# Performance work log

Hardware: AMD Instinct MI355X
Metric: run time of the kernel (lower is better)

## Reference

```python
import jax, jax.numpy as jnp
import numpy as np

B, QL, KL, D, H = 2, 512, 8192, 1024, 8
HD = D // H  # head dim = 128


def setup_inputs() -> dict:
    key = jax.random.key(0)
    ks = jax.random.split(key, 12)
    s = 0.02
    return {
        "inputs_q": jax.random.normal(ks[0], (B, QL, D), jnp.float32),
        "inputs_k": jax.random.normal(ks[1], (B, KL, D), jnp.float32),
        "inputs_v": jax.random.normal(ks[2], (B, KL, D), jnp.float32),
        "attention_mask": jax.random.randint(ks[3], (B, QL, KL), 0, 2).astype(bool),
        "Wq": jax.random.normal(ks[4], (D, D), jnp.float32) * s,
        "bq": jnp.zeros((D,), jnp.float32),
        "Wk": jax.random.normal(ks[5], (D, D), jnp.float32) * s,
        "bk": jnp.zeros((D,), jnp.float32),
        "Wv": jax.random.normal(ks[6], (D, D), jnp.float32) * s,
        "bv": jnp.zeros((D,), jnp.float32),
        "Wf": jax.random.normal(ks[7], (D, D), jnp.float32) * s,
        "bf": jnp.zeros((D,), jnp.float32),
    }


def reference(inputs_q, inputs_k, inputs_v, attention_mask, Wq, bq, Wk, bk, Wv, bv, Wf, bf):
    # Projections (torch Linear: x @ W.T + b)
    q = inputs_q @ Wq.T + bq  # [B, QL, D]
    k = inputs_k @ Wk.T + bk  # [B, KL, D]
    v = inputs_v @ Wv.T + bv  # [B, KL, D]

    q = q.reshape(B, QL, H, HD)
    k = k.reshape(B, KL, H, HD)
    v = v.reshape(B, KL, H, HD)

    # scores [B, H, QL, KL]
    scores = jnp.einsum("bqhd,bkhd->bhqk", q, k)
    scale = 1.0 / np.sqrt(HD).astype(np.float32)
    scores = scores * scale
    large_k = jnp.float32(1e30)
    scores = jnp.where(attention_mask[:, None, :, :], scores, -large_k)

    probs = jax.nn.softmax(scores, axis=-1)
    # note: original calls self.dropout(normalized) but discards the result -> no-op

    summed = jnp.einsum("bhqk,bkhd->bqhd", probs, v).reshape(B, QL, H * HD)

    # wipe rows whose mask is all zero
    wipe = jnp.all(~attention_mask, axis=2, keepdims=True)  # [B, QL, 1]
    summed = jnp.where(wipe, jnp.zeros_like(summed), summed)

    return summed @ Wf.T + bf
```

## Files before the change

### kernel.cpp

```cpp
#include <hip/hip_runtime.h>
#include <hip/hip_bf16.h>
#include <math.h>

typedef __attribute__((ext_vector_type(4))) float fx4;
typedef __attribute__((ext_vector_type(4))) short sx4;
typedef __attribute__((ext_vector_type(8))) short sx8;
typedef unsigned long long u64;

#define MFMA16(a, b, c) __builtin_amdgcn_mfma_f32_16x16x16bf16_1k(a, b, c, 0, 0, 0)
#define MFMA32(a, b, c) __builtin_amdgcn_mfma_f32_16x16x32_bf16(a, b, c, 0, 0, 0)

__device__ __forceinline__ unsigned short f2bf(float f) {
  unsigned int u = __float_as_uint(f);
  return (unsigned short)((u + 0x7fffu + ((u >> 16) & 1u)) >> 16);
}

__device__ __forceinline__ unsigned cvtpk(float lo, float hi) {
  unsigned r;
  asm("v_cvt_pk_bf16_f32 %0, %1, %2" : "=v"(r) : "v"(lo), "v"(hi));
  return r;
}

typedef const __attribute__((address_space(1))) char* gc1p;
typedef __attribute__((address_space(3))) char* lc3p;
__device__ __forceinline__ void glds16(const void* g, const void* lds_uniform) {
  gc1p gp = (gc1p)(unsigned long long)(uintptr_t)g;
  lc3p lp = (lc3p)(unsigned)__builtin_amdgcn_readfirstlane((int)(unsigned)(uintptr_t)lds_uniform);
  __builtin_amdgcn_global_load_lds(gp, lp, 16, 0, 0);
}

__global__ __launch_bounds__(256) void k_prep(
    const float* __restrict__ Wq, const float* __restrict__ Wk,
    const float* __restrict__ Wv, const float* __restrict__ Wf,
    const int* __restrict__ mask, short* cwq, short* cwk, short* cwv,
    short* cwf, u64* __restrict__ mb) {
  __shared__ unsigned char nib[4][256];
  const int bx = blockIdx.x;
  const int t = threadIdx.x;
  if (bx >= 256) {
    const int mrow0 = (bx - 256) * 4;
#pragma unroll
    for (int j = 0; j < 4; j++) {
      const int4 m = *(const int4*)(mask + (size_t)(mrow0 + j) * 1024 + t * 4);
      nib[j][t] = (unsigned char)((m.x != 0) | ((m.y != 0) << 1) |
                                  ((m.z != 0) << 2) | ((m.w != 0) << 3));
    }
    __syncthreads();
    if (t < 64) {
      const int j = t >> 4, i = t & 15;
      u64 wv = 0;
#pragma unroll
      for (int k = 0; k < 16; k++)
        wv |= (u64)(nib[j][i * 16 + k] & 0xF) << (4 * k);
      mb[(size_t)(mrow0 + j) * 16 + i] = wv;
    }
    return;
  }
  const int seg = bx >> 6;
  const float* s = seg == 0 ? Wq : seg == 1 ? Wk : seg == 2 ? Wv : Wf;
  short* d = seg == 0 ? cwq : seg == 1 ? cwk : seg == 2 ? cwv : cwf;
  const size_t base = (size_t)(bx & 63) * 16384;
#pragma unroll
  for (int it = 0; it < 4; it++) {
    const size_t i = base + (size_t)it * 4096 + (size_t)t * 16;
    const fx4 a0 = *(const fx4*)(s + i);
    const fx4 a1 = *(const fx4*)(s + i + 4);
    const fx4 a2 = *(const fx4*)(s + i + 8);
    const fx4 a3 = *(const fx4*)(s + i + 12);
    sx8 o0, o1;
    o0[0] = (short)f2bf(a0[0]); o0[1] = (short)f2bf(a0[1]);
    o0[2] = (short)f2bf(a0[2]); o0[3] = (short)f2bf(a0[3]);
    o0[4] = (short)f2bf(a1[0]); o0[5] = (short)f2bf(a1[1]);
    o0[6] = (short)f2bf(a1[2]); o0[7] = (short)f2bf(a1[3]);
    o1[0] = (short)f2bf(a2[0]); o1[1] = (short)f2bf(a2[1]);
    o1[2] = (short)f2bf(a2[2]); o1[3] = (short)f2bf(a2[3]);
    o1[4] = (short)f2bf(a3[0]); o1[5] = (short)f2bf(a3[1]);
    o1[6] = (short)f2bf(a3[2]); o1[7] = (short)f2bf(a3[3]);
    *(sx8*)(d + i) = o0;
    *(sx8*)(d + i + 8) = o1;
  }
}

template <int MODE, int MT, int AF32>
__device__ __forceinline__ void gemm_body(short* sA, short* sB,
                                          const void* __restrict__ Aptr,
                                          const short* __restrict__ Bw,
                                          const float* __restrict__ bias,
                                          void* __restrict__ Cptr, int M, int N,
                                          int K, float alpha, int bx) {
  const int t = threadIdx.x;
  const int lane = t & 63;
  const int w = t >> 6;
  const int quad = lane >> 4;
  const int l16 = lane & 15;
  const int x7 = l16 & 7;
  int m0, n0;
  if (M >= 8192) {
    const int ml = bx & 7, nn = (bx >> 3) & 7, mh = bx >> 6;
    m0 = (mh * 8 + ml) * MT;
    n0 = nn << 7;
  } else {
    const int ntile = N >> 7;
    n0 = (bx % ntile) << 7;
    m0 = (bx / ntile) * MT;
  }
  constexpr int NI = (MT == 128) ? 4 : 2;
  constexpr int NJ = (MT == 128) ? 4 : 2;
  const int wm = (MT == 128) ? ((w >> 1) << 6) : 0;
  const int wn = (MT == 128) ? ((w & 1) << 6) : (w << 5);
  const fx4 fzero = {0.f, 0.f, 0.f, 0.f};
  fx4 acc[4][NI];
#pragma unroll
  for (int i = 0; i < 4; i++)
#pragma unroll
    for (int j = 0; j < NI; j++) acc[i][j] = fzero;

  const int srow = lane >> 3;
  const int scb = lane & 7;
  const float* Af = (const float*)Aptr;
  const short* Ab = (const short*)Aptr;
  fx4 ra[NJ][2];

  if (AF32) {
#pragma unroll
    for (int j = 0; j < NJ; j++) {
      const int rbase = (MT == 128) ? (w * 32 + j * 8) : (j * 32 + w * 8);
      const int row = rbase + srow;
      const int cb = scb ^ (row & 7);
      const float* src = Af + (size_t)(m0 + row) * K + cb * 8;
      ra[j][0] = *(const fx4*)src;
      ra[j][1] = *(const fx4*)(src + 4);
    }
  } else {
#pragma unroll
    for (int j = 0; j < NJ; j++) {
      const int rbase = (MT == 128) ? (w * 32 + j * 8) : (j * 32 + w * 8);
      const int row = rbase + srow;
      const int cb = scb ^ (row & 7);
      glds16(Ab + (size_t)(m0 + row) * K + cb * 8, &sA[rbase * 64]);
    }
  }
#pragma unroll
  for (int j = 0; j < 4; j++) {
    const int row = w * 32 + j * 8 + srow;
    const int cb = scb ^ (row & 7);
    glds16(Bw + (size_t)(n0 + row) * K + cb * 8, &sB[(w * 32 + j * 8) * 64]);
  }
  if (AF32) {
#pragma unroll
    for (int j = 0; j < NJ; j++) {
      const int rbase = (MT == 128) ? (w * 32 + j * 8) : (j * 32 + w * 8);
      sx8 o;
      unsigned* ou = (unsigned*)&o;
      ou[0] = cvtpk(ra[j][0][0], ra[j][0][1]);
      ou[1] = cvtpk(ra[j][0][2], ra[j][0][3]);
      ou[2] = cvtpk(ra[j][1][0], ra[j][1][1]);
      ou[3] = cvtpk(ra[j][1][2], ra[j][1][3]);
      *(sx8*)(&sA[rbase * 64 + lane * 8]) = o;
    }
  }
  __syncthreads();

  int buf = 0;
  for (int k0 = 0; k0 < K; k0 += 64) {
    const int nb = buf ^ 1;
    const bool more = (k0 + 64 < K);
    if (more) {
#pragma unroll
      for (int j = 0; j < 4; j++) {
        const int row = w * 32 + j * 8 + srow;
        const int cb = scb ^ (row & 7);
        glds16(Bw + (size_t)(n0 + row) * K + (k0 + 64) + cb * 8,
               &sB[nb * 8192 + (w * 32 + j * 8) * 64]);
      }
      if (AF32) {
#pragma unroll
        for (int j = 0; j < NJ; j++) {
          const int rbase = (MT == 128) ? (w * 32 + j * 8) : (j * 32 + w * 8);
          const int row = rbase + srow;
          const int cb = scb ^ (row & 7);
          const float* src = Af + (size_t)(m0 + row) * K + (k0 + 64) + cb * 8;
          ra[j][0] = *(const fx4*)src;
          ra[j][1] = *(const fx4*)(src + 4);
        }
      } else {
#pragma unroll
        for (int j = 0; j < NJ; j++) {
          const int rbase = (MT == 128) ? (w * 32 + j * 8) : (j * 32 + w * 8);
          const int row = rbase + srow;
          const int cb = scb ^ (row & 7);
          glds16(Ab + (size_t)(m0 + row) * K + (k0 + 64) + cb * 8,
                 &sA[nb * 8192 + rbase * 64]);
        }
      }
    }
    const short* pA = sA + buf * 8192;
    const short* pB = sB + buf * 8192;
#pragma unroll
    for (int kc = 0; kc < 2; kc++) {
      const int cbp = ((kc * 4 + quad) ^ x7) * 8;
      sx8 fa[4], fb[NI];
#pragma unroll
      for (int i = 0; i < 4; i++)
        fa[i] = *(const sx8*)(&pA[(wm + i * 16 + l16) * 64 + cbp]);
#pragma unroll
      for (int i = 0; i < NI; i++)
        fb[i] = *(const sx8*)(&pB[(wn + i * 16 + l16) * 64 + cbp]);
#pragma unroll
      for (int mi = 0; mi < 4; mi++)
#pragma unroll
        for (int ni = 0; ni < NI; ni++)
          acc[mi][ni] = MFMA32(fa[mi], fb[ni], acc[mi][ni]);
    }
    if (AF32 && more) {
#pragma unroll
      for (int j = 0; j < NJ; j++) {
        const int rbase = (MT == 128) ? (w * 32 + j * 8) : (j * 32 + w * 8);
        sx8 o;
        unsigned* ou = (unsigned*)&o;
        ou[0] = cvtpk(ra[j][0][0], ra[j][0][1]);
        ou[1] = cvtpk(ra[j][0][2], ra[j][0][3]);
        ou[2] = cvtpk(ra[j][1][0], ra[j][1][1]);
        ou[3] = cvtpk(ra[j][1][2], ra[j][1][3]);
        *(sx8*)(&sA[nb * 8192 + rbase * 64 + lane * 8]) = o;
      }
    }
    __syncthreads();
    buf = nb;
  }
#pragma unroll
  for (int ni = 0; ni < NI; ni++) {
    const int col = n0 + wn + ni * 16 + l16;
    const float bval = bias[col];
    if (MODE == 2) {
#pragma unroll
      for (int mi = 0; mi < 4; mi++) {
        const int rowb = m0 + wm + mi * 16 + quad * 4;
        const int bb = rowb >> 13;
        const int kl = (rowb & 8191) ^ ((col & 8) ? 4 : 0);
        sx4 pkv;
#pragma unroll
        for (int r = 0; r < 4; r++) pkv[r] = (short)f2bf(acc[mi][ni][r] + bval);
        *(sx4*)((unsigned short*)Cptr + ((size_t)bb * 1024 + col) * 8192 + kl) = pkv;
      }
    } else {
#pragma unroll
      for (int mi = 0; mi < 4; mi++)
#pragma unroll
        for (int r = 0; r < 4; r++) {
          const int row = m0 + wm + mi * 16 + quad * 4 + r;
          const float v = (acc[mi][ni][r] + bval) * alpha;
          if (MODE == 1) ((float*)Cptr)[(size_t)row * N + col] = v;
          else ((unsigned short*)Cptr)[(size_t)row * N + col] = f2bf(v);
        }
    }
  }
}

__global__ __launch_bounds__(256) void k_proj(
    const float* __restrict__ ink, const short* __restrict__ cwk,
    const float* __restrict__ bk, short* __restrict__ Kp,
    const float* __restrict__ inv, const short* __restrict__ cwv,
    const float* __restrict__ bv, short* __restrict__ Vt,
    const float* __restrict__ inq, const short* __restrict__ cwq,
    const float* __restrict__ bq, short* __restrict__ Qp, float alpha_q) {
  __shared__ __align__(16) short smem[32768];
  const int bx = blockIdx.x;
  if (bx < 1024)
    gemm_body<0, 128, 1>(smem, smem + 16384, ink, cwk, bk, Kp, 16384, 1024,
                         1024, 1.f, bx);
  else if (bx < 2048)
    gemm_body<2, 128, 1>(smem, smem + 16384, inv, cwv, bv, Vt, 16384, 1024,
                         1024, 1.f, bx - 1024);
  else
    gemm_body<0, 64, 1>(smem, smem + 16384, inq, cwq, bq, Qp, 1024, 1024, 1024,
                        alpha_q, bx - 2048);
}

__global__ __launch_bounds__(256) void k_gemm_out(const short* __restrict__ summed,
                                                  const short* __restrict__ cwf,
                                                  const float* __restrict__ bf,
                                                  float* __restrict__ out) {
  __shared__ __align__(16) short smem[32768];
  gemm_body<1, 64, 0>(smem, smem + 16384, summed, cwf, bf, out, 1024, 1024,
                      1024, 1.f, blockIdx.x);
}

__global__ __launch_bounds__(256, 4) void k_attn(const short* __restrict__ Qp,
                                                 const short* __restrict__ Kp,
                                                 const short* __restrict__ Vt,
                                                 const u64* __restrict__ mb,
                                                 float* __restrict__ ml,
                                                 float* __restrict__ Op) {
  __shared__ __align__(16) short sK[8192];
  __shared__ __align__(16) short sV[8192];
  const int x = blockIdx.x;
  const int gl = x & 7;
  const int qt = (x >> 3) & 7;
  const int gh = x >> 6;
  const int g = gh * 8 + gl;
  const int s = g & 7;
  const int h = (g >> 3) & 7;
  const int b = g >> 6;
  const int li = ((b * 8 + h) * 8 + qt) * 8 + s;
  const int t = threadIdx.x;
  const int lane = t & 63;
  const int w = t >> 6;
  const int quad = lane >> 4;
  const int l16 = lane & 15;
  const int x7 = l16 & 7;
  const int q0 = qt << 6;
  const fx4 fzero = {0.f, 0.f, 0.f, 0.f};

  const short* qbase = Qp + (size_t)(b * 512 + q0 + w * 16 + l16) * 1024 + h * 128;
  sx8 aq[4];
#pragma unroll
  for (int kc = 0; kc < 4; kc++) aq[kc] = *(const sx8*)(qbase + kc * 32 + quad * 8);

  fx4 Ot[8];
#pragma unroll
  for (int d = 0; d < 8; d++) Ot[d] = fzero;
  float lsum = 0.f;

  const short* kbase = Kp + (size_t)(b * 8192 + s * 1024) * 1024 + h * 128;
  const short* vbase = Vt + (size_t)(b * 1024 + h * 128) * 8192 + s * 1024;
  const u64* wdp = mb + (size_t)(b * 512 + q0 + w * 16 + l16) * 128 + s * 16;
  const int srow4 = lane >> 4, scb16 = lane & 15;
  const int srow8 = lane >> 3, scb8 = lane & 7;
  const int h4 = ((quad & 1) ^ ((l16 >> 3) & 1)) * 4;

  for (int kt = 0; kt < 16; kt++) {
    __syncthreads();
#pragma unroll
    for (int j = 0; j < 4; j++) {
      const int row = (w * 4 + j) * 4 + srow4;
      const int cb = scb16 ^ (row & 7);
      glds16(kbase + (size_t)(kt * 64 + row) * 1024 + cb * 8, &sK[(w * 4 + j) * 512]);
    }
#pragma unroll
    for (int j = 0; j < 4; j++) {
      const int row = (w * 4 + j) * 8 + srow8;
      const int cb = scb8 ^ (row & 7);
      glds16(vbase + (size_t)row * 8192 + kt * 64 + cb * 8, &sV[(w * 4 + j) * 512]);
    }
    const u64 wd = wdp[kt];
    __syncthreads();
    const unsigned lo = (unsigned)wd, hi = (unsigned)(wd >> 32);
    sx4 pk[4];
#pragma unroll
    for (int nt = 0; nt < 4; nt++) {
      fx4 a = fzero;
#pragma unroll
      for (int kc = 0; kc < 4; kc++) {
        const sx8 kf = *(const sx8*)(&sK[(nt * 16 + l16) * 128 + ((kc * 4 + quad) ^ x7) * 8]);
        a = MFMA32(kf, aq[kc], a);
      }
      const unsigned bits = (nt & 2) ? hi : lo;
      const int sh = (nt & 1) * 16 + quad * 4;
      float pv[4];
#pragma unroll
      for (int r = 0; r < 4; r++) {
        const float e = __builtin_amdgcn_exp2f(a[r]);
        pv[r] = ((bits >> (sh + r)) & 1u) ? e : 0.f;
        lsum += pv[r];
      }
      sx4 pko;
      ((unsigned*)&pko)[0] = __builtin_amdgcn_perm(
          __float_as_uint(pv[1]) + 0x8000u, __float_as_uint(pv[0]) + 0x8000u, 0x07060302u);
      ((unsigned*)&pko)[1] = __builtin_amdgcn_perm(
          __float_as_uint(pv[3]) + 0x8000u, __float_as_uint(pv[2]) + 0x8000u, 0x07060302u);
      pk[nt] = pko;
    }
#pragma unroll
    for (int dt = 0; dt < 8; dt++) {
      fx4 o = Ot[dt];
#pragma unroll
      for (int nt = 0; nt < 4; nt++) {
        const int cb = (2 * nt + (quad >> 1)) ^ x7;
        const sx4 vf = *(const sx4*)(&sV[(dt * 16 + l16) * 64 + cb * 8 + h4]);
        o = MFMA16(vf, pk[nt], o);
      }
      Ot[dt] = o;
    }
  }
  lsum += __shfl_xor(lsum, 16, 64);
  lsum += __shfl_xor(lsum, 32, 64);
  if (lane < 16) ml[(size_t)li * 64 + w * 16 + l16] = lsum;
  float* ob = Op + (size_t)li * 8192 + (w * 16 + l16) * 128 + quad * 4;
#pragma unroll
  for (int dt = 0; dt < 8; dt++) *(fx4*)(ob + dt * 16) = Ot[dt];
}

__global__ __launch_bounds__(256) void k_combine(const float* __restrict__ ml,
                                                 const float* __restrict__ Op,
                                                 short* __restrict__ summed) {
  const int bx = blockIdx.x;
  const int xc = bx >> 1;
  const int dh = (bx & 1) * 64;
  const int qt = xc & 7;
  const int h = (xc >> 3) & 7;
  const int b = xc >> 6;
  const int t = threadIdx.x;
  const int row = t >> 2;
  const int dg = dh + (t & 3) * 16;
  float L = 0.f;
#pragma unroll
  for (int s = 0; s < 8; s++) L += ml[(size_t)(xc * 8 + s) * 64 + row];
  float o[16];
#pragma unroll
  for (int i = 0; i < 16; i++) o[i] = 0.f;
  if (L != 0.f) {
#pragma unroll
    for (int s = 0; s < 8; s++) {
      const float* src = Op + (size_t)(xc * 8 + s) * 8192 + row * 128 + dg;
#pragma unroll
      for (int i = 0; i < 4; i++) {
        const fx4 v = *(const fx4*)(src + i * 4);
        o[i * 4 + 0] += v[0]; o[i * 4 + 1] += v[1];
        o[i * 4 + 2] += v[2]; o[i * 4 + 3] += v[3];
      }
    }
    const float inv = 1.f / L;
#pragma unroll
    for (int i = 0; i < 16; i++) o[i] *= inv;
  }
  short* dst = summed + (size_t)(b * 512 + qt * 64 + row) * 1024 + h * 128 + dg;
#pragma unroll
  for (int i = 0; i < 2; i++) {
    sx8 pkv;
#pragma unroll
    for (int j = 0; j < 8; j++) pkv[j] = (short)f2bf(o[i * 8 + j]);
    *(sx8*)(dst + i * 8) = pkv;
  }
}

extern "C" void kernel_launch(void* const* d_in, const int* in_sizes, int n_in,
                              void* d_out, int out_size, void* d_ws, size_t ws_size,
                              hipStream_t stream) {
  (void)in_sizes; (void)n_in; (void)out_size; (void)ws_size;
  const float* inq = (const float*)d_in[0];
  const float* ink = (const float*)d_in[1];
  const float* inv = (const float*)d_in[2];
  const int* mask = (const int*)d_in[3];
  const float* Wq = (const float*)d_in[4];
  const float* bq = (const float*)d_in[5];
  const float* Wk = (const float*)d_in[6];
  const float* bk = (const float*)d_in[7];
  const float* Wv = (const float*)d_in[8];
  const float* bv = (const float*)d_in[9];
  const float* Wf = (const float*)d_in[10];
  const float* bf = (const float*)d_in[11];

  char* ws = (char*)d_ws;
  short* Vt = (short*)(ws + 0);
  short* Kp = (short*)(ws + 33554432);
  float* Op = (float*)(ws + 67108864);
  short* cwq = (short*)(ws + 102760448);
  short* cwk = (short*)(ws + 104857600);
  short* cwv = (short*)(ws + 106954752);
  short* cwf = (short*)(ws + 109051904);
  short* Qp = (short*)(ws + 111149056);
  short* summed = (short*)(ws + 113246208);
  u64* mb = (u64*)(ws + 115343360);
  float* ml = (float*)(ws + 116391936);

  const float alpha_q = 0.12751757f;

  k_prep<<<2304, 256, 0, stream>>>(Wq, Wk, Wv, Wf, mask, cwq, cwk, cwv, cwf, mb);
  k_proj<<<2176, 256, 0, stream>>>(ink, cwk, bk, Kp, inv, cwv, bv, Vt, inq, cwq,
                                   bq, Qp, alpha_q);
  k_attn<<<1024, 256, 0, stream>>>(Qp, Kp, Vt, mb, ml, Op);
  k_combine<<<256, 256, 0, stream>>>(ml, Op, summed);
  k_gemm_out<<<128, 256, 0, stream>>>(summed, cwf, bf, (float*)d_out);
}
```

Before: 380.8 us.

## Pipeline projection GEMM with two-deep A prefetch and move mask packing into projection kernel

The projection GEMM gets a software pipeline: fp32 A tiles are prefetched two steps ahead into a double register slot, with explicit vmcnt waits and sched barriers replacing __syncthreads. Mask bit-packing moves from the prep kernel into extra blocks of the projection launch so it overlaps with GEMM work, and k_proj gets a launch-bounds occupancy hint. The attention kernel raises wave priority around its MFMA sections. The aim is to hide global-load latency and shorten the prep kernel, at the cost of more registers and hand-written wait counts that must match the load count exactly.

```diff
diff --git a/kernel.cpp b/kernel.cpp
--- a/kernel.cpp
+++ b/kernel.cpp
@@ -31,31 +31,10 @@
 
 __global__ __launch_bounds__(256) void k_prep(
     const float* __restrict__ Wq, const float* __restrict__ Wk,
-    const float* __restrict__ Wv, const float* __restrict__ Wf,
-    const int* __restrict__ mask, short* cwq, short* cwk, short* cwv,
-    short* cwf, u64* __restrict__ mb) {
-  __shared__ unsigned char nib[4][256];
+    const float* __restrict__ Wv, const float* __restrict__ Wf, short* cwq,
+    short* cwk, short* cwv, short* cwf) {
   const int bx = blockIdx.x;
   const int t = threadIdx.x;
-  if (bx >= 256) {
-    const int mrow0 = (bx - 256) * 4;
-#pragma unroll
-    for (int j = 0; j < 4; j++) {
-      const int4 m = *(const int4*)(mask + (size_t)(mrow0 + j) * 1024 + t * 4);
-      nib[j][t] = (unsigned char)((m.x != 0) | ((m.y != 0) << 1) |
-                                  ((m.z != 0) << 2) | ((m.w != 0) << 3));
-    }
-    __syncthreads();
-    if (t < 64) {
-      const int j = t >> 4, i = t & 15;
-      u64 wv = 0;
-#pragma unroll
-      for (int k = 0; k < 16; k++)
-        wv |= (u64)(nib[j][i * 16 + k] & 0xF) << (4 * k);
-      mb[(size_t)(mrow0 + j) * 16 + i] = wv;
-    }
-    return;
-  }
   const int seg = bx >> 6;
   const float* s = seg == 0 ? Wq : seg == 1 ? Wk : seg == 2 ? Wv : Wf;
   short* d = seg == 0 ? cwq : seg == 1 ? cwk : seg == 2 ? cwv : cwf;
@@ -81,16 +60,18 @@
   }
 }
 
-template <int MODE, int MT, int AF32>
-__device__ __forceinline__ void gemm_body(short* sA, short* sB,
-                                          const void* __restrict__ Aptr,
+template <int MODE, int MT>
+__device__ __forceinline__ void gemm_pipe(short* sA, short* sB,
+                                          const float* __restrict__ Af,
                                           const short* __restrict__ Bw,
                                           const float* __restrict__ bias,
                                           void* __restrict__ Cptr, int M, int N,
-                                          int K, float alpha, int bx) {
-  const int t = threadIdx.x;
-  const int lane = t & 63;
-  const int w = t >> 6;
+                                          float alpha, int bx) {
+  constexpr int K = 1024;
+  constexpr int NT = 16;
+  const int tid = threadIdx.x;
+  const int lane = tid & 63;
+  const int w = tid >> 6;
   const int quad = lane >> 4;
   const int l16 = lane & 15;
   const int x7 = l16 & 7;
@@ -117,28 +98,152 @@
 
   const int srow = lane >> 3;
   const int scb = lane & 7;
-  const float* Af = (const float*)Aptr;
-  const short* Ab = (const short*)Aptr;
-  fx4 ra[NJ][2];
-
-  if (AF32) {
+  fx4 ra[2][NJ][2];
+
+  auto ISSUE_B = [&](int t) {
+#pragma unroll
+    for (int j = 0; j < 4; j++) {
+      const int row = w * 32 + j * 8 + srow;
+      const int cb = scb ^ (row & 7);
+      glds16(Bw + (size_t)(n0 + row) * K + t * 64 + cb * 8,
+             &sB[(t & 1) * 8192 + (w * 32 + j * 8) * 64]);
+    }
+  };
+  auto ISSUE_A = [&](int t, int slot) {
 #pragma unroll
     for (int j = 0; j < NJ; j++) {
       const int rbase = (MT == 128) ? (w * 32 + j * 8) : (j * 32 + w * 8);
       const int row = rbase + srow;
       const int cb = scb ^ (row & 7);
-      const float* src = Af + (size_t)(m0 + row) * K + cb * 8;
-      ra[j][0] = *(const fx4*)src;
-      ra[j][1] = *(const fx4*)(src + 4);
-    }
-  } else {
+      const float* src = Af + (size_t)(m0 + row) * K + t * 64 + cb * 8;
+      ra[slot][j][0] = *(const fx4*)src;
+      ra[slot][j][1] = *(const fx4*)(src + 4);
+    }
+  };
+  auto CVT_A = [&](int t, int slot) {
 #pragma unroll
     for (int j = 0; j < NJ; j++) {
       const int rbase = (MT == 128) ? (w * 32 + j * 8) : (j * 32 + w * 8);
-      const int row = rbase + srow;
-      const int cb = scb ^ (row & 7);
-      glds16(Ab + (size_t)(m0 + row) * K + cb * 8, &sA[rbase * 64]);
-    }
+      sx8 o;
+      unsigned* ou = (unsigned*)&o;
+      ou[0] = cvtpk(ra[slot][j][0][0], ra[slot][j][0][1]);
+      ou[1] = cvtpk(ra[slot][j][0][2], ra[slot][j][0][3]);
+      ou[2] = cvtpk(ra[slot][j][1][0], ra[slot][j][1][1]);
+      ou[3] = cvtpk(ra[slot][j][1][2], ra[slot][j][1][3]);
+      *(sx8*)(&sA[(t & 1) * 8192 + rbase * 64 + lane * 8]) = o;
+    }
+  };
+  auto COMPUTE = [&](int t) {
+    const short* pA = sA + (t & 1) * 8192;
+    const short* pB = sB + (t & 1) * 8192;
+#pragma unroll
+    for (int kc = 0; kc < 2; kc++) {
+      const int cbp = ((kc * 4 + quad) ^ x7) * 8;
+      sx8 fa[4], fb[NI];
+#pragma unroll
+      for (int i = 0; i < 4; i++)
+        fa[i] = *(const sx8*)(&pA[(wm + i * 16 + l16) * 64 + cbp]);
+#pragma unroll
+      for (int i = 0; i < NI; i++)
+        fb[i] = *(const sx8*)(&pB[(wn + i * 16 + l16) * 64 + cbp]);
+#pragma unroll
+      for (int mi = 0; mi < 4; mi++)
+#pragma unroll
+        for (int ni = 0; ni < NI; ni++)
+          acc[mi][ni] = MFMA32(fa[mi], fb[ni], acc[mi][ni]);
+    }
+  };
+
+  ISSUE_B(0);
+  __builtin_amdgcn_sched_barrier(0);
+  ISSUE_A(0, 0);
+  __builtin_amdgcn_sched_barrier(0);
+  ISSUE_B(1);
+  __builtin_amdgcn_sched_barrier(0);
+  ISSUE_A(1, 1);
+  __builtin_amdgcn_sched_barrier(0);
+  CVT_A(0, 0);
+  asm volatile("s_waitcnt lgkmcnt(0)\n\ts_barrier" ::: "memory");
+
+#pragma unroll
+  for (int t = 0; t < NT; ++t) {
+    if (t + 1 < NT) ISSUE_B(t + 1);
+    __builtin_amdgcn_sched_barrier(0);
+    if (t + 2 < NT) ISSUE_A(t + 2, t & 1);
+    __builtin_amdgcn_sched_barrier(0);
+    COMPUTE(t);
+    if (t + 1 < NT) CVT_A(t + 1, (t + 1) & 1);
+    if (t + 2 < NT) {
+      if (MT == 128)
+        asm volatile("s_waitcnt vmcnt(8) lgkmcnt(0)\n\ts_barrier" ::: "memory");
+      else
+        asm volatile("s_waitcnt vmcnt(4) lgkmcnt(0)\n\ts_barrier" ::: "memory");
+    } else if (t + 1 < NT) {
+      asm volatile("s_waitcnt vmcnt(0) lgkmcnt(0)\n\ts_barrier" ::: "memory");
+    }
+  }
+#pragma unroll
+  for (int ni = 0; ni < NI; ni++) {
+    const int col = n0 + wn + ni * 16 + l16;
+    const float bval = bias[col];
+    if (MODE == 2) {
+#pragma unroll
+      for (int mi = 0; mi < 4; mi++) {
+        const int rowb = m0 + wm + mi * 16 + quad * 4;
+        const int bb = rowb >> 13;
+        const int kl = (rowb & 8191) ^ ((col & 8) ? 4 : 0);
+        sx4 pkv;
+#pragma unroll
+        for (int r = 0; r < 4; r++) pkv[r] = (short)f2bf(acc[mi][ni][r] + bval);
+        *(sx4*)((unsigned short*)Cptr + ((size_t)bb * 1024 + col) * 8192 + kl) = pkv;
+      }
+    } else {
+#pragma unroll
+      for (int mi = 0; mi < 4; mi++)
+#pragma unroll
+        for (int r = 0; r < 4; r++) {
+          const int row = m0 + wm + mi * 16 + quad * 4 + r;
+          const float v = (acc[mi][ni][r] + bval) * alpha;
+          ((unsigned short*)Cptr)[(size_t)row * N + col] = f2bf(v);
+        }
+    }
+  }
+}
+
+__device__ __forceinline__ void gemm_out_body(short* sA, short* sB,
+                                              const short* __restrict__ A,
+                                              const short* __restrict__ Bw,
+                                              const float* __restrict__ bias,
+                                              float* __restrict__ Cptr, int N,
+                                              int K, int bx) {
+  constexpr int MT = 64;
+  const int tid = threadIdx.x;
+  const int lane = tid & 63;
+  const int w = tid >> 6;
+  const int quad = lane >> 4;
+  const int l16 = lane & 15;
+  const int x7 = l16 & 7;
+  const int ntile = N >> 7;
+  const int n0 = (bx % ntile) << 7;
+  const int m0 = (bx / ntile) * MT;
+  constexpr int NI = 2;
+  const int wm = 0;
+  const int wn = w << 5;
+  const fx4 fzero = {0.f, 0.f, 0.f, 0.f};
+  fx4 acc[4][NI];
+#pragma unroll
+  for (int i = 0; i < 4; i++)
+#pragma unroll
+    for (int j = 0; j < NI; j++) acc[i][j] = fzero;
+  const int srow = lane >> 3;
+  const int scb = lane & 7;
+
+#pragma unroll
+  for (int j = 0; j < 2; j++) {
+    const int rbase = j * 32 + w * 8;
+    const int row = rbase + srow;
+    const int cb = scb ^ (row & 7);
+    glds16(A + (size_t)(m0 + row) * K + cb * 8, &sA[rbase * 64]);
   }
 #pragma unroll
   for (int j = 0; j < 4; j++) {
@@ -146,26 +251,12 @@
     const int cb = scb ^ (row & 7);
     glds16(Bw + (size_t)(n0 + row) * K + cb * 8, &sB[(w * 32 + j * 8) * 64]);
   }
-  if (AF32) {
-#pragma unroll
-    for (int j = 0; j < NJ; j++) {
-      const int rbase = (MT == 128) ? (w * 32 + j * 8) : (j * 32 + w * 8);
-      sx8 o;
-      unsigned* ou = (unsigned*)&o;
-      ou[0] = cvtpk(ra[j][0][0], ra[j][0][1]);
-      ou[1] = cvtpk(ra[j][0][2], ra[j][0][3]);
-      ou[2] = cvtpk(ra[j][1][0], ra[j][1][1]);
-      ou[3] = cvtpk(ra[j][1][2], ra[j][1][3]);
-      *(sx8*)(&sA[rbase * 64 + lane * 8]) = o;
-    }
-  }
   __syncthreads();
 
   int buf = 0;
   for (int k0 = 0; k0 < K; k0 += 64) {
     const int nb = buf ^ 1;
-    const bool more = (k0 + 64 < K);
-    if (more) {
+    if (k0 + 64 < K) {
 #pragma unroll
       for (int j = 0; j < 4; j++) {
         const int row = w * 32 + j * 8 + srow;
@@ -173,25 +264,13 @@
         glds16(Bw + (size_t)(n0 + row) * K + (k0 + 64) + cb * 8,
                &sB[nb * 8192 + (w * 32 + j * 8) * 64]);
       }
-      if (AF32) {
-#pragma unroll
-        for (int j = 0; j < NJ; j++) {
-          const int rbase = (MT == 128) ? (w * 32 + j * 8) : (j * 32 + w * 8);
-          const int row = rbase + srow;
-          const int cb = scb ^ (row & 7);
-          const float* src = Af + (size_t)(m0 + row) * K + (k0 + 64) + cb * 8;
-          ra[j][0] = *(const fx4*)src;
-          ra[j][1] = *(const fx4*)(src + 4);
-        }
-      } else {
-#pragma unroll
-        for (int j = 0; j < NJ; j++) {
-          const int rbase = (MT == 128) ? (w * 32 + j * 8) : (j * 32 + w * 8);
-          const int row = rbase + srow;
-          const int cb = scb ^ (row & 7);
-          glds16(Ab + (size_t)(m0 + row) * K + (k0 + 64) + cb * 8,
-                 &sA[nb * 8192 + rbase * 64]);
-        }
+#pragma unroll
+      for (int j = 0; j < 2; j++) {
+        const int rbase = j * 32 + w * 8;
+        const int row = rbase + srow;
+        const int cb = scb ^ (row & 7);
+        glds16(A + (size_t)(m0 + row) * K + (k0 + 64) + cb * 8,
+               &sA[nb * 8192 + rbase * 64]);
       }
     }
     const short* pA = sA + buf * 8192;
@@ -212,19 +291,6 @@
         for (int ni = 0; ni < NI; ni++)
           acc[mi][ni] = MFMA32(fa[mi], fb[ni], acc[mi][ni]);
     }
-    if (AF32 && more) {
-#pragma unroll
-      for (int j = 0; j < NJ; j++) {
-        const int rbase = (MT == 128) ? (w * 32 + j * 8) : (j * 32 + w * 8);
-        sx8 o;
-        unsigned* ou = (unsigned*)&o;
-        ou[0] = cvtpk(ra[j][0][0], ra[j][0][1]);
-        ou[1] = cvtpk(ra[j][0][2], ra[j][0][3]);
-        ou[2] = cvtpk(ra[j][1][0], ra[j][1][1]);
-        ou[3] = cvtpk(ra[j][1][2], ra[j][1][3]);
-        *(sx8*)(&sA[nb * 8192 + rbase * 64 + lane * 8]) = o;
-      }
-    }
     __syncthreads();
     buf = nb;
   }
@@ -232,49 +298,56 @@
   for (int ni = 0; ni < NI; ni++) {
     const int col = n0 + wn + ni * 16 + l16;
     const float bval = bias[col];
-    if (MODE == 2) {
-#pragma unroll
-      for (int mi = 0; mi < 4; mi++) {
-        const int rowb = m0 + wm + mi * 16 + quad * 4;
-        const int bb = rowb >> 13;
-        const int kl = (rowb & 8191) ^ ((col & 8) ? 4 : 0);
-        sx4 pkv;
-#pragma unroll
-        for (int r = 0; r < 4; r++) pkv[r] = (short)f2bf(acc[mi][ni][r] + bval);
-        *(sx4*)((unsigned short*)Cptr + ((size_t)bb * 1024 + col) * 8192 + kl) = pkv;
-      }
-    } else {
-#pragma unroll
-      for (int mi = 0; mi < 4; mi++)
-#pragma unroll
-        for (int r = 0; r < 4; r++) {
-          const int row = m0 + wm + mi * 16 + quad * 4 + r;
-          const float v = (acc[mi][ni][r] + bval) * alpha;
-          if (MODE == 1) ((float*)Cptr)[(size_t)row * N + col] = v;
-          else ((unsigned short*)Cptr)[(size_t)row * N + col] = f2bf(v);
-        }
-    }
-  }
-}
-
-__global__ __launch_bounds__(256) void k_proj(
+#pragma unroll
+    for (int mi = 0; mi < 4; mi++)
+#pragma unroll
+      for (int r = 0; r < 4; r++) {
+        const int row = m0 + wm + mi * 16 + quad * 4 + r;
+        Cptr[(size_t)row * N + col] = acc[mi][ni][r] + bval;
+      }
+  }
+}
+
+__global__ __launch_bounds__(256, 2) void k_proj(
     const float* __restrict__ ink, const short* __restrict__ cwk,
     const float* __restrict__ bk, short* __restrict__ Kp,
     const float* __restrict__ inv, const short* __restrict__ cwv,
     const float* __restrict__ bv, short* __restrict__ Vt,
     const float* __restrict__ inq, const short* __restrict__ cwq,
-    const float* __restrict__ bq, short* __restrict__ Qp, float alpha_q) {
+    const float* __restrict__ bq, short* __restrict__ Qp, float alpha_q,
+    const int* __restrict__ mask, u64* __restrict__ mb) {
   __shared__ __align__(16) short smem[32768];
   const int bx = blockIdx.x;
+  if (bx >= 2176) {
+    unsigned char(*nib)[256] = (unsigned char(*)[256])smem;
+    const int t = threadIdx.x;
+    const int mrow0 = (bx - 2176) * 4;
+#pragma unroll
+    for (int j = 0; j < 4; j++) {
+      const int4 m = *(const int4*)(mask + (size_t)(mrow0 + j) * 1024 + t * 4);
+      nib[j][t] = (unsigned char)((m.x != 0) | ((m.y != 0) << 1) |
+                                  ((m.z != 0) << 2) | ((m.w != 0) << 3));
+    }
+    __syncthreads();
+    if (t < 64) {
+      const int j = t >> 4, i = t & 15;
+      u64 wv = 0;
+#pragma unroll
+      for (int k = 0; k < 16; k++)
+        wv |= (u64)(nib[j][i * 16 + k] & 0xF) << (4 * k);
+      mb[(size_t)(mrow0 + j) * 16 + i] = wv;
+    }
+    return;
+  }
   if (bx < 1024)
-    gemm_body<0, 128, 1>(smem, smem + 16384, ink, cwk, bk, Kp, 16384, 1024,
-                         1024, 1.f, bx);
+    gemm_pipe<0, 128>(smem, smem + 16384, ink, cwk, bk, Kp, 16384, 1024, 1.f,
+                      bx);
   else if (bx < 2048)
-    gemm_body<2, 128, 1>(smem, smem + 16384, inv, cwv, bv, Vt, 16384, 1024,
-                         1024, 1.f, bx - 1024);
+    gemm_pipe<2, 128>(smem, smem + 16384, inv, cwv, bv, Vt, 16384, 1024, 1.f,
+                      bx - 1024);
   else
-    gemm_body<0, 64, 1>(smem, smem + 16384, inq, cwq, bq, Qp, 1024, 1024, 1024,
-                        alpha_q, bx - 2048);
+    gemm_pipe<0, 64>(smem, smem + 16384, inq, cwq, bq, Qp, 1024, 1024, alpha_q,
+                     bx - 2048);
 }
 
 __global__ __launch_bounds__(256) void k_gemm_out(const short* __restrict__ summed,
@@ -282,8 +355,8 @@
                                                   const float* __restrict__ bf,
                                                   float* __restrict__ out) {
   __shared__ __align__(16) short smem[32768];
-  gemm_body<1, 64, 0>(smem, smem + 16384, summed, cwf, bf, out, 1024, 1024,
-                      1024, 1.f, blockIdx.x);
+  gemm_out_body(smem, smem + 16384, summed, cwf, bf, out, 1024, 1024,
+                blockIdx.x);
 }
 
 __global__ __launch_bounds__(256, 4) void k_attn(const short* __restrict__ Qp,
@@ -350,11 +423,13 @@
 #pragma unroll
     for (int nt = 0; nt < 4; nt++) {
       fx4 a = fzero;
+      __builtin_amdgcn_s_setprio(1);
 #pragma unroll
       for (int kc = 0; kc < 4; kc++) {
         const sx8 kf = *(const sx8*)(&sK[(nt * 16 + l16) * 128 + ((kc * 4 + quad) ^ x7) * 8]);
         a = MFMA32(kf, aq[kc], a);
       }
+      __builtin_amdgcn_s_setprio(0);
       const unsigned bits = (nt & 2) ? hi : lo;
       const int sh = (nt & 1) * 16 + quad * 4;
       float pv[4];
@@ -371,6 +446,7 @@
           __float_as_uint(pv[3]) + 0x8000u, __float_as_uint(pv[2]) + 0x8000u, 0x07060302u);
       pk[nt] = pko;
     }
+    __builtin_amdgcn_s_setprio(1);
 #pragma unroll
     for (int dt = 0; dt < 8; dt++) {
       fx4 o = Ot[dt];
@@ -382,6 +458,7 @@
       }
       Ot[dt] = o;
     }
+    __builtin_amdgcn_s_setprio(0);
   }
   lsum += __shfl_xor(lsum, 16, 64);
   lsum += __shfl_xor(lsum, 32, 64);
@@ -466,9 +543,9 @@
 
   const float alpha_q = 0.12751757f;
 
-  k_prep<<<2304, 256, 0, stream>>>(Wq, Wk, Wv, Wf, mask, cwq, cwk, cwv, cwf, mb);
-  k_proj<<<2176, 256, 0, stream>>>(ink, cwk, bk, Kp, inv, cwv, bv, Vt, inq, cwq,
-                                   bq, Qp, alpha_q);
+  k_prep<<<256, 256, 0, stream>>>(Wq, Wk, Wv, Wf, cwq, cwk, cwv, cwf);
+  k_proj<<<4224, 256, 0, stream>>>(ink, cwk, bk, Kp, inv, cwv, bv, Vt, inq, cwq,
+                                   bq, Qp, alpha_q, mask, mb);
   k_attn<<<1024, 256, 0, stream>>>(Qp, Kp, Vt, mb, ml, Op);
   k_combine<<<256, 256, 0, stream>>>(ml, Op, summed);
   k_gemm_out<<<128, 256, 0, stream>>>(summed, cwf, bf, (float*)d_out);
```

Result: faster. 351.5 us (-7.7%).
